# Kernel optimization log

Measured on AMD Instinct MI355X. Metric: run time of the kernel, lower is better.

The kernel has to match this reference:

```python
import jax, jax.numpy as jnp
import numpy as np


def setup_inputs() -> dict:
    key = jax.random.key(0)
    kK, kQ = jax.random.split(key)
    B, S, D = 8, 2048, 512
    K = jax.random.normal(kK, (B, S, D), dtype=jnp.float32)
    Q = jax.random.normal(kQ, (B, S, D), dtype=jnp.float32)
    return {"K": K, "Q": Q}


def reference(K, Q):
    # K: [B, S_k, D], Q: [B, S_q, D]
    S_q = Q.shape[1]
    S_k = K.shape[1]
    # Causal mask: -inf strictly above the diagonal (k=1), as in np.triu(..., k=1)
    mask = jnp.where(jnp.triu(jnp.ones((S_q, S_k), dtype=bool), k=1), -jnp.inf, 0.0).astype(jnp.float32)
    # NOTE: original scales by sqrt(window_size_keys) (seq len), and adds mask BEFORE scaling.
    logits = (jnp.einsum('bqd,bkd->bqk', Q, K) + mask) / jnp.sqrt(jnp.float32(S_k))
    return jax.nn.softmax(logits, axis=-1)
```

## Files before the change

### kernel.cpp

```cpp
#include <hip/hip_runtime.h>
#include <hip/hip_bf16.h>
#include <math.h>

#define B_SZ 8
#define SEQ 2048
#define DIM 512

typedef __attribute__((ext_vector_type(8))) short bf16x8;
typedef __attribute__((ext_vector_type(8))) unsigned short u16x8;
typedef __attribute__((ext_vector_type(4))) float f32x4;

#define GLOBAL_AS __attribute__((address_space(1)))
#define LDS_AS __attribute__((address_space(3)))

__device__ __forceinline__ unsigned short f2bf(float f) {
    unsigned int u = __builtin_bit_cast(unsigned int, f);
    u += 0x7fffu + ((u >> 16) & 1u);
    return (unsigned short)(u >> 16);
}

__device__ __forceinline__ void load_lds16(const void* g, void* l) {
    __builtin_amdgcn_global_load_lds((const GLOBAL_AS unsigned int*)g,
                                     (LDS_AS unsigned int*)l, 16, 0, 0);
}

__global__ __launch_bounds__(256)
void convert_kernel(const float* __restrict__ Qs, const float* __restrict__ Ks,
                    unsigned short* __restrict__ Qd, unsigned short* __restrict__ Kd) {
    const float* src = blockIdx.y ? Qs : Ks;
    unsigned short* dst = blockIdx.y ? Qd : Kd;
    int i = blockIdx.x * 256 + threadIdx.x;
    const float4* s = (const float4*)src;
    float4 a = s[2 * i];
    float4 b = s[2 * i + 1];
    u16x8 o;
    o[0] = f2bf(a.x); o[1] = f2bf(a.y); o[2] = f2bf(a.z); o[3] = f2bf(a.w);
    o[4] = f2bf(b.x); o[5] = f2bf(b.y); o[6] = f2bf(b.z); o[7] = f2bf(b.w);
    ((u16x8*)dst)[i] = o;
}

#define BM 128
#define BK 32
__global__ __launch_bounds__(256)
void logits_exp(const unsigned short* __restrict__ Qb, const unsigned short* __restrict__ Kb,
                float* __restrict__ out, float* __restrict__ partials) {
    const int tk = blockIdx.x, tq = blockIdx.y, b = blockIdx.z;
    const int t = threadIdx.x;
    float* outb = out + (size_t)b * SEQ * SEQ;

    if (tk > tq) {
        float4 z = {0.f, 0.f, 0.f, 0.f};
        float4* o = (float4*)(outb + (size_t)(tq * BM) * SEQ + tk * BM);
        const int c4 = t & 31;
        const int r0 = t >> 5;
#pragma unroll
        for (int r = 0; r < BM; r += 8)
            o[(size_t)(r + r0) * (SEQ / 4) + c4] = z;
        return;
    }

    __shared__ __align__(16) unsigned short a_lds[BM * BK];
    __shared__ __align__(16) unsigned short b_lds[BM * BK];

    const int wave = t >> 6;
    const int lane = t & 63;
    const int l16 = lane & 15;
    const int quad = lane >> 4;
    const int wm = wave >> 1;
    const int wn = wave & 1;

    const unsigned short* Qrow = Qb + ((size_t)b * SEQ + (size_t)tq * BM) * DIM;
    const unsigned short* Krow = Kb + ((size_t)b * SEQ + (size_t)tk * BM) * DIM;

    const int sr = lane >> 2;
    const int kg = lane & 3;

    f32x4 acc[4][4];
#pragma unroll
    for (int i = 0; i < 4; i++)
#pragma unroll
        for (int j = 0; j < 4; j++) acc[i][j] = (f32x4){0.f, 0.f, 0.f, 0.f};

    for (int k0 = 0; k0 < DIM; k0 += BK) {
#pragma unroll
        for (int j = wave; j < 8; j += 4) {
            int row = j * 16 + sr;
            load_lds16(Qrow + (size_t)row * DIM + k0 + kg * 8, &a_lds[(j * 16) * BK]);
            load_lds16(Krow + (size_t)row * DIM + k0 + kg * 8, &b_lds[(j * 16) * BK]);
        }
        __syncthreads();

        bf16x8 af[4], bf[4];
#pragma unroll
        for (int mi = 0; mi < 4; mi++)
            af[mi] = *(const bf16x8*)&a_lds[(wm * 64 + mi * 16 + l16) * BK + quad * 8];
#pragma unroll
        for (int ni = 0; ni < 4; ni++)
            bf[ni] = *(const bf16x8*)&b_lds[(wn * 64 + ni * 16 + l16) * BK + quad * 8];
#pragma unroll
        for (int mi = 0; mi < 4; mi++)
#pragma unroll
            for (int ni = 0; ni < 4; ni++)
                acc[mi][ni] = __builtin_amdgcn_mfma_f32_16x16x32_bf16(af[mi], bf[ni], acc[mi][ni], 0, 0, 0);
        __syncthreads();
    }

    const float scale = 0.02209708691207961f;
    const bool diag = (tk == tq);
#pragma unroll
    for (int mi = 0; mi < 4; mi++) {
        const int rowb = tq * BM + wm * 64 + mi * 16 + quad * 4;
#pragma unroll
        for (int r = 0; r < 4; r++) {
            const int row = rowb + r;
            float psum = 0.f;
#pragma unroll
            for (int ni = 0; ni < 4; ni++) {
                const int col = tk * BM + wn * 64 + ni * 16 + l16;
                float e = __expf(acc[mi][ni][r] * scale);
                e = (!diag || col <= row) ? e : 0.f;
                psum += e;
                outb[(size_t)row * SEQ + col] = e;
            }
            psum += __shfl_xor(psum, 1);
            psum += __shfl_xor(psum, 2);
            psum += __shfl_xor(psum, 4);
            psum += __shfl_xor(psum, 8);
            if (l16 == 0)
                partials[((size_t)b * SEQ + row) * 32 + tk * 2 + wn] = psum;
        }
    }
}

__global__ __launch_bounds__(256)
void rescale_kernel(float* __restrict__ out, const float* __restrict__ partials) {
    const int q = blockIdx.x & (SEQ - 1);
    const int b = blockIdx.x >> 11;
    const int t = threadIdx.x;
    const int lane = t & 63;
    const int tqt = q >> 7;
    const int nslots = (tqt + 1) * 2;

    float v = 0.f;
    if (lane < nslots) v = partials[((size_t)(b * SEQ + q)) * 32 + lane];
    v += __shfl_xor(v, 1);
    v += __shfl_xor(v, 2);
    v += __shfl_xor(v, 4);
    v += __shfl_xor(v, 8);
    v += __shfl_xor(v, 16);
    const float inv = 1.0f / __shfl(v, 0);

    float4* row = (float4*)(out + ((size_t)b * SEQ + q) * SEQ);
    const int n4 = (tqt + 1) * 32;
    for (int i = t; i < n4; i += 256) {
        float4 e = row[i];
        e.x *= inv; e.y *= inv; e.z *= inv; e.w *= inv;
        row[i] = e;
    }
}

extern "C" void kernel_launch(void* const* d_in, const int* in_sizes, int n_in,
                              void* d_out, int out_size, void* d_ws, size_t ws_size,
                              hipStream_t stream) {
    const float* Kp = (const float*)d_in[0];
    const float* Qp = (const float*)d_in[1];
    float* out = (float*)d_out;

    const size_t nElem = (size_t)B_SZ * SEQ * DIM;
    unsigned short* Qbf = (unsigned short*)d_ws;
    unsigned short* Kbf = Qbf + nElem;
    float* partials = (float*)(Kbf + nElem);

    convert_kernel<<<dim3((unsigned)(nElem / 2048), 2), dim3(256), 0, stream>>>(Qp, Kp, Qbf, Kbf);
    logits_exp<<<dim3(SEQ / BM, SEQ / BM, B_SZ), dim3(256), 0, stream>>>(Qbf, Kbf, out, partials);
    rescale_kernel<<<dim3(B_SZ * SEQ), dim3(256), 0, stream>>>(out, partials);
}
```

Before: 253.2 us.

## Launch only lower-triangular tiles and zero upper region in rescale pass

```diff
diff --git a/kernel.cpp b/kernel.cpp
--- a/kernel.cpp
+++ b/kernel.cpp
@@ -5,6 +5,8 @@
 #define B_SZ 8
 #define SEQ 2048
 #define DIM 512
+#define NT (SEQ / 128)
+#define NTRI (NT * (NT + 1) / 2)
 
 typedef __attribute__((ext_vector_type(8))) short bf16x8;
 typedef __attribute__((ext_vector_type(8))) unsigned short u16x8;
@@ -29,14 +31,18 @@
                     unsigned short* __restrict__ Qd, unsigned short* __restrict__ Kd) {
     const float* src = blockIdx.y ? Qs : Ks;
     unsigned short* dst = blockIdx.y ? Qd : Kd;
-    int i = blockIdx.x * 256 + threadIdx.x;
+    const int base = blockIdx.x * (256 * 8) + threadIdx.x;
     const float4* s = (const float4*)src;
-    float4 a = s[2 * i];
-    float4 b = s[2 * i + 1];
-    u16x8 o;
-    o[0] = f2bf(a.x); o[1] = f2bf(a.y); o[2] = f2bf(a.z); o[3] = f2bf(a.w);
-    o[4] = f2bf(b.x); o[5] = f2bf(b.y); o[6] = f2bf(b.z); o[7] = f2bf(b.w);
-    ((u16x8*)dst)[i] = o;
+#pragma unroll
+    for (int j = 0; j < 8; j++) {
+        int i = base + j * 256;
+        float4 a = s[2 * i];
+        float4 b = s[2 * i + 1];
+        u16x8 o;
+        o[0] = f2bf(a.x); o[1] = f2bf(a.y); o[2] = f2bf(a.z); o[3] = f2bf(a.w);
+        o[4] = f2bf(b.x); o[5] = f2bf(b.y); o[6] = f2bf(b.z); o[7] = f2bf(b.w);
+        ((u16x8*)dst)[i] = o;
+    }
 }
 
 #define BM 128
@@ -44,24 +50,17 @@
 __global__ __launch_bounds__(256)
 void logits_exp(const unsigned short* __restrict__ Qb, const unsigned short* __restrict__ Kb,
                 float* __restrict__ out, float* __restrict__ partials) {
-    const int tk = blockIdx.x, tq = blockIdx.y, b = blockIdx.z;
-    const int t = threadIdx.x;
-    float* outb = out + (size_t)b * SEQ * SEQ;
-
-    if (tk > tq) {
-        float4 z = {0.f, 0.f, 0.f, 0.f};
-        float4* o = (float4*)(outb + (size_t)(tq * BM) * SEQ + tk * BM);
-        const int c4 = t & 31;
-        const int r0 = t >> 5;
-#pragma unroll
-        for (int r = 0; r < BM; r += 8)
-            o[(size_t)(r + r0) * (SEQ / 4) + c4] = z;
-        return;
-    }
+    const int tid = blockIdx.x;
+    const int b = blockIdx.y;
+    int tq = (int)((sqrtf(8.f * (float)tid + 1.f) - 1.f) * 0.5f);
+    while ((tq + 1) * (tq + 2) / 2 <= tid) tq++;
+    while (tq * (tq + 1) / 2 > tid) tq--;
+    const int tk = tid - tq * (tq + 1) / 2;
 
     __shared__ __align__(16) unsigned short a_lds[BM * BK];
     __shared__ __align__(16) unsigned short b_lds[BM * BK];
 
+    const int t = threadIdx.x;
     const int wave = t >> 6;
     const int lane = t & 63;
     const int l16 = lane & 15;
@@ -107,6 +106,7 @@
 
     const float scale = 0.02209708691207961f;
     const bool diag = (tk == tq);
+    float* outb = out + (size_t)b * SEQ * SEQ;
 #pragma unroll
     for (int mi = 0; mi < 4; mi++) {
         const int rowb = tq * BM + wm * 64 + mi * 16 + quad * 4;
@@ -134,28 +134,36 @@
 
 __global__ __launch_bounds__(256)
 void rescale_kernel(float* __restrict__ out, const float* __restrict__ partials) {
-    const int q = blockIdx.x & (SEQ - 1);
-    const int b = blockIdx.x >> 11;
-    const int t = threadIdx.x;
-    const int lane = t & 63;
-    const int tqt = q >> 7;
-    const int nslots = (tqt + 1) * 2;
-
-    float v = 0.f;
-    if (lane < nslots) v = partials[((size_t)(b * SEQ + q)) * 32 + lane];
-    v += __shfl_xor(v, 1);
-    v += __shfl_xor(v, 2);
-    v += __shfl_xor(v, 4);
-    v += __shfl_xor(v, 8);
-    v += __shfl_xor(v, 16);
-    const float inv = 1.0f / __shfl(v, 0);
-
-    float4* row = (float4*)(out + ((size_t)b * SEQ + q) * SEQ);
-    const int n4 = (tqt + 1) * 32;
-    for (int i = t; i < n4; i += 256) {
-        float4 e = row[i];
-        e.x *= inv; e.y *= inv; e.z *= inv; e.w *= inv;
-        row[i] = e;
+    const int rowbase = blockIdx.x * 8;
+    const int wave = threadIdx.x >> 6;
+    const int lane = threadIdx.x & 63;
+#pragma unroll
+    for (int rr = 0; rr < 2; rr++) {
+        const int grow = rowbase + wave * 2 + rr;
+        const int q = grow & (SEQ - 1);
+        const int tqt = q >> 7;
+        const int nslots = (tqt + 1) * 2;
+        float v = (lane < nslots) ? partials[(size_t)grow * 32 + lane] : 0.f;
+        v += __shfl_xor(v, 1);
+        v += __shfl_xor(v, 2);
+        v += __shfl_xor(v, 4);
+        v += __shfl_xor(v, 8);
+        v += __shfl_xor(v, 16);
+        v += __shfl_xor(v, 32);
+        const float inv = 1.0f / v;
+        const int n4 = (tqt + 1) * 32;
+        float4* row = (float4*)(out + (size_t)grow * SEQ);
+#pragma unroll
+        for (int j = 0; j < 8; j++) {
+            const int i = lane + j * 64;
+            if (i < n4) {
+                float4 e = row[i];
+                e.x *= inv; e.y *= inv; e.z *= inv; e.w *= inv;
+                row[i] = e;
+            } else {
+                row[i] = (float4){0.f, 0.f, 0.f, 0.f};
+            }
+        }
     }
 }
 
@@ -171,7 +179,7 @@
     unsigned short* Kbf = Qbf + nElem;
     float* partials = (float*)(Kbf + nElem);
 
-    convert_kernel<<<dim3((unsigned)(nElem / 2048), 2), dim3(256), 0, stream>>>(Qp, Kp, Qbf, Kbf);
-    logits_exp<<<dim3(SEQ / BM, SEQ / BM, B_SZ), dim3(256), 0, stream>>>(Qbf, Kbf, out, partials);
-    rescale_kernel<<<dim3(B_SZ * SEQ), dim3(256), 0, stream>>>(out, partials);
+    convert_kernel<<<dim3(512, 2), dim3(256), 0, stream>>>(Qp, Kp, Qbf, Kbf);
+    logits_exp<<<dim3(NTRI, B_SZ), dim3(256), 0, stream>>>(Qbf, Kbf, out, partials);
+    rescale_kernel<<<dim3(B_SZ * SEQ / 8), dim3(256), 0, stream>>>(out, partials);
 }
```

Result: no change. 250.6 us (-1.0%).
